# Performance work log

Measured on AMD Instinct MI355X. Metric: run time of the kernel, lower is better.

## Reference

```python
import jax, jax.numpy as jnp
import numpy as np

N_NODES = 50000
N_G_EDGES = 400000
N_LG_EDGES = 600000
N_HEADS = 4
OUT_FEATS = 64
EPS = 0.001


def segment_mean(x, seg_ids, num_segments):
    s = jax.ops.segment_sum(x, seg_ids, num_segments=num_segments)
    cnt = jax.ops.segment_sum(jnp.ones((x.shape[0],), x.dtype), seg_ids, num_segments=num_segments)
    return s / jnp.maximum(cnt, 1.0)[(...,) + (None,) * (x.ndim - 1)]


def setup_inputs() -> dict:
    key = jax.random.key(0)
    ks = jax.random.split(key, 12)
    return {
        'atomic_number': jax.random.randint(ks[0], (N_NODES,), 0, 4),
        'g_src': jax.random.randint(ks[1], (N_G_EDGES,), 0, N_NODES),
        'g_dst': jax.random.randint(ks[2], (N_G_EDGES,), 0, N_NODES),
        'lg_src': jax.random.randint(ks[3], (N_LG_EDGES,), 0, N_G_EDGES),
        'lg_dst': jax.random.randint(ks[4], (N_LG_EDGES,), 0, N_G_EDGES),
        'costheta': jax.random.uniform(ks[5], (N_LG_EDGES,), jnp.float32),
        'dnr': jax.random.uniform(ks[6], (N_LG_EDGES,), jnp.float32),
        'a': jax.random.uniform(ks[7], (N_HEADS,), jnp.float32),
        'b': jax.random.uniform(ks[8], (N_HEADS,), jnp.float32),
        'c': jax.random.uniform(ks[9], (N_HEADS,), jnp.float32),
        'd': jax.random.uniform(ks[10], (N_HEADS,), jnp.float32),
        'value_table': jax.random.normal(ks[11], (4, OUT_FEATS * N_HEADS), jnp.float32),
    }


def reference(atomic_number, g_src, g_dst, lg_src, lg_dst, costheta, dnr, a, b, c, d, value_table):
    # send_k_src: per g-edge atomic numbers of endpoints
    k_src = atomic_number[g_src]  # (E_g,)
    k_dst = atomic_number[g_dst]  # (E_g,)

    # masked symmetry key on line-graph edges (edge pair: lg_src -> lg_dst, g-edge indices)
    ka = k_src[lg_src]
    kc = k_dst[lg_dst]
    kb = k_dst[lg_src]
    peripheral = (ka == kc).astype(jnp.int32)
    central = ((kb == ka) & (kb == kc)).astype(jnp.int32)
    sym_key = peripheral * 2 + central  # (E_lg,), values in {0,1,2,3}

    # value embedding lookup -> (E_lg, F, H)
    asv = value_table[sym_key].reshape(N_LG_EDGES, OUT_FEATS, N_HEADS)

    # angular / radial symmetry per head
    ct = jnp.clip(costheta, -EPS, EPS)
    theta = jnp.arccos(ct)[:, None]  # (E_lg, 1)
    B = b % jnp.pi
    angular = ((jnp.cos(a[None, :] * theta + B[None, :]) + 1.0) / 2.0) ** c[None, :]  # (E_lg, H)
    radial = jnp.exp(-d[None, :] * (dnr[:, None] ** 2))  # (E_lg, H)
    spatial = radial * angular

    sv = asv * spatial[:, None, :]  # (E_lg, F, H)

    # reverse line-graph mean: aggregate lg edges by their (original) source lg-node = g-edge
    w_edge = segment_mean(sv, lg_src, N_G_EDGES)  # (E_g, F, H)
    # reverse graph mean: aggregate g edges by their (original) source node
    w_node = segment_mean(w_edge, g_src, N_NODES)  # (N, F, H)

    return jnp.sum(w_node, axis=-1)  # (N, F)
```

## Files before the change

### kernel.cpp

```cpp
#include <hip/hip_runtime.h>
#include <math.h>

typedef unsigned long long u64;
typedef unsigned int u32;
typedef unsigned short u16;
typedef unsigned char u8;

#define N_NODES    50000
#define N_G_EDGES  400000
#define N_LG_EDGES 600000
#define OUT_FEATS  64
#define EPSV       0.001f
#define PI_F       3.14159265358979323846f
#define HPI_F      1.57079632679489662f
#define FXSCALE    512.0f
#define INV_FXSCALE (1.0f/512.0f)

#define SB_N    256
#define EPB1    2344
#define LH_B0   256
#define LG_CH   16
#define LG_BINS 50000
#define LG_W    12500
#define LG_EPC  37500
#define GH_B0   384
#define GH_CH   16
#define GH_W    12500
#define GH_EPC  25000
#define PK_B0   400
#define PK_GPB  3572
#define K1_GRID 512

#define WID   1564
#define NLSB  256
#define NPB   196
#define SPB   (NPB*4)
#define CAP2  2816


__global__ __launch_bounds__(1024) void k1(const int* __restrict__ an,
                                           const int* __restrict__ gsrc,
                                           const int* __restrict__ gdst,
                                           const int* __restrict__ lgsrc,
                                           const int* __restrict__ lgdst,
                                           const float* __restrict__ costheta,
                                           const float* __restrict__ dnr,
                                           u8*  __restrict__ kk8,
                                           u32* __restrict__ clg,
                                           u32* __restrict__ cg,
                                           uint4* __restrict__ srecs,
                                           u32* __restrict__ prefT1) {
    __shared__ u32 smem[12800];
    const int tid = threadIdx.x;
    const int bid = blockIdx.x;

    if (bid < SB_N) {
        uint4* rec = (uint4*)smem;
        u32* lcnt = smem + 9600;
        u32* pref = smem + 9872;
        if (tid < 256) lcnt[tid] = 0u;
        __syncthreads();
        const int e0 = bid * EPB1;
        const int e1 = (e0 + EPB1 < N_LG_EDGES) ? e0 + EPB1 : N_LG_EDGES;
        u32 meta[3]; uint4 val[3];
#pragma unroll
        for (int it = 0; it < 3; ++it) {
            meta[it] = 0u;
            int e = e0 + it * 1024 + tid;
            if (e < e1) {
                int ls = lgsrc[e];
                int ld = lgdst[e];
                float ct = costheta[e];
                float dn = dnr[e];
                u32 bk = (u32)ls / WID;
                u32 rank = atomicAdd(&lcnt[bk], 1u);
                val[it] = make_uint4(__float_as_uint(ct), __float_as_uint(dn),
                                     (u32)ld, (u32)ls);
                meta[it] = 0x80000000u | (rank << 8) | bk;
            }
        }
        __syncthreads();
        if (tid < 256) pref[tid + 1] = lcnt[tid];
        if (tid == 0) pref[0] = 0u;
        __syncthreads();
        for (int off = 1; off < 256; off <<= 1) {
            u32 add = 0;
            if (tid < 256 && tid >= off) add = pref[tid - off + 1];
            __syncthreads();
            if (tid < 256) pref[tid + 1] += add;
            __syncthreads();
        }
#pragma unroll
        for (int it = 0; it < 3; ++it) {
            if (meta[it] & 0x80000000u) {
                u32 bk = meta[it] & 0xffu;
                u32 pos = pref[bk] + ((meta[it] >> 8) & 0x1fffu);
                rec[pos] = val[it];
            }
        }
        __syncthreads();
        const u32 btot = pref[256];
        uint4* dst = srecs + (size_t)bid * EPB1;
        for (u32 i = tid; i < btot; i += 1024) dst[i] = rec[i];
        if (tid <= 256) prefT1[bid * 257 + tid] = pref[tid];
    } else if (bid < GH_B0) {
        const int bid2 = bid - LH_B0;
        const int cc = bid2 & 15, r = bid2 >> 4;
        const int lo = r * LG_BINS;
        for (int w = tid; w < LG_W; w += 1024) smem[w] = 0u;
        __syncthreads();
        const int s0 = cc * LG_EPC;
        for (int e = s0 + tid; e < s0 + LG_EPC; e += 1024) {
            unsigned lb = (unsigned)(lgsrc[e] - lo);
            if (lb < (unsigned)LG_BINS)
                atomicAdd(&smem[lb >> 2], 1u << (8 * (lb & 3)));
        }
        __syncthreads();
        u32* dst = clg + (size_t)bid2 * LG_W;
        for (int w = tid; w < LG_W; w += 1024) dst[w] = smem[w];
    } else if (bid < PK_B0) {
        const int cc = bid - GH_B0;
        for (int w = tid; w < GH_W; w += 1024) smem[w] = 0u;
        __syncthreads();
        const int s0 = cc * GH_EPC;
        for (int g = s0 + tid; g < s0 + GH_EPC; g += 1024) {
            int n = gsrc[g];
            atomicAdd(&smem[n >> 2], 1u << (8 * (n & 3)));
        }
        __syncthreads();
        u32* dst = cg + (size_t)cc * GH_W;
        for (int w = tid; w < GH_W; w += 1024) dst[w] = smem[w];
    } else {
        const int g0 = (bid - PK_B0) * PK_GPB;
        const int g1 = (g0 + PK_GPB < N_G_EDGES) ? g0 + PK_GPB : N_G_EDGES;
        for (int g = g0 + tid; g < g1; g += 1024)
            kk8[g] = (u8)(an[gsrc[g]] | (an[gdst[g]] << 4));
    }
}

__global__ __launch_bounds__(1024) void k2(const int* __restrict__ gsrc,
                                           const u8*  __restrict__ kk8,
                                           const u32* __restrict__ clg,
                                           const uint4* __restrict__ srecs,
                                           const u32* __restrict__ prefT1,
                                           const float* __restrict__ pa,
                                           const float* __restrict__ pb,
                                           const float* __restrict__ pc,
                                           const float* __restrict__ pd,
                                           uint4* __restrict__ mrecs,
                                           u32* __restrict__ prefT2) {
    __shared__ uint4 rec[CAP2];
    __shared__ float invw[WID];
    __shared__ u16   nodew[WID];
    __shared__ u8    kkw[WID];
    __shared__ u32 sstart[256];
    __shared__ u32 spref[257];
    __shared__ u32 lcnt[256];
    __shared__ u32 pref2[257];
    const int tid = threadIdx.x;
    const int b = blockIdx.x;
    const int lo = b * WID;

    for (int i = tid; i < WID; i += 1024) {
        int ls = lo + i;
        float inv = 0.0f; u16 nd = 0; u8 kw = 0;
        if (ls < N_G_EDGES) {
            int r = ls / LG_BINS, lb = ls - r * LG_BINS;
            int w = lb >> 2, sh = 8 * (lb & 3);
            const u32* base = clg + (size_t)(r * LG_CH) * LG_W + w;
            u32 c = 0;
#pragma unroll
            for (int cc = 0; cc < LG_CH; ++cc) c += (base[(size_t)cc * LG_W] >> sh) & 0xffu;
            inv = 1.0f / (float)(c < 1u ? 1u : c);
            nd = (u16)gsrc[ls];
            kw = kk8[ls];
        }
        invw[i] = inv; nodew[i] = nd; kkw[i] = kw;
    }
    if (tid < 256) {
        u32 a = prefT1[tid * 257 + b];
        u32 c2 = prefT1[tid * 257 + b + 1];
        sstart[tid] = a; spref[tid + 1] = c2 - a; lcnt[tid] = 0u;
    }
    if (tid == 0) spref[0] = 0u;
    __syncthreads();
    for (int off = 1; off < 256; off <<= 1) {
        u32 add = 0;
        if (tid < 256 && tid >= off) add = spref[tid - off + 1];
        __syncthreads();
        if (tid < 256) spref[tid + 1] += add;
        __syncthreads();
    }
    const u32 total = spref[256];

    float A0[4], A1[4], A2[4], DD[4];
#pragma unroll
    for (int h = 0; h < 4; ++h) {
        float a = pa[h], B = fmodf(pb[h], PI_F), c = pc[h], d = pd[h];
        float K = a * HPI_F + B;
        float ck = cosf(K), sk = sinf(K);
        float u0 = 0.5f * (1.0f + ck);
        float f0 = powf(u0, c);
        float g1 = (-0.5f * a * sk) / u0;
        float u2 = -0.25f * a * a * ck;
        float g2 = u2 / u0 - 0.5f * g1 * g1;
        A0[h] = f0;
        A1[h] = f0 * c * g1;
        A2[h] = f0 * (c * g2 + 0.5f * c * c * g1 * g1);
        DD[h] = d;
    }

    u64 qv[3]; u32 mv[3];
#pragma unroll
    for (int it = 0; it < 3; ++it) {
        mv[it] = 0u;
        u32 i = (u32)(it * 1024 + tid);
        if (i < total) {
            int l2 = 0, h2 = 256;
            while (h2 - l2 > 1) {
                int mid = (l2 + h2) >> 1;
                if (spref[mid] <= i) l2 = mid; else h2 = mid;
            }
            uint4 r4 = srecs[(size_t)l2 * EPB1 + sstart[l2] + (i - spref[l2])];
            float ct = __uint_as_float(r4.x);
            float dn = __uint_as_float(r4.y);
            u32 ld = r4.z;
            int li = (int)r4.w - lo;
            float inv = invw[li];
            int node = (int)nodew[li];
            u32 kw = kkw[li];
            int ka = (int)(kw & 0xfu);
            int kb = (int)(kw >> 4);
            int kd = kk8[ld] >> 4;
            int key = ((ka == kd) ? 2 : 0) + ((kb == ka && kb == kd) ? 1 : 0);
            ct = fminf(fmaxf(ct, -EPSV), EPSV);
            float del = -ct;
            float dn2 = dn * dn;
            float s = inv * FXSCALE;
            u64 q = 0;
#pragma unroll
            for (int h = 0; h < 4; ++h) {
                float ang = A0[h] + del * (A1[h] + del * A2[h]);
                float rad = __expf(-DD[h] * dn2);
                q |= (u64)(u32)(ang * rad * s + 0.5f) << (16 * h);
            }
            u32 nb = (u32)node / NPB;
            u32 slot = ((u32)node - nb * NPB) * 4u + (u32)key;
            u32 rank = atomicAdd(&lcnt[nb], 1u);
            qv[it] = q;
            mv[it] = 0x80000000u | (rank << 18) | (nb << 10) | slot;
        }
    }
    __syncthreads();
    if (tid < 256) pref2[tid + 1] = lcnt[tid];
    if (tid == 0) pref2[0] = 0u;
    __syncthreads();
    for (int off = 1; off < 256; off <<= 1) {
        u32 add = 0;
        if (tid < 256 && tid >= off) add = pref2[tid - off + 1];
        __syncthreads();
        if (tid < 256) pref2[tid + 1] += add;
        __syncthreads();
    }
#pragma unroll
    for (int it = 0; it < 3; ++it) {
        if (mv[it] & 0x80000000u) {
            u32 nb = (mv[it] >> 10) & 0xffu;
            u32 pos = pref2[nb] + ((mv[it] >> 18) & 0x1fffu);
            if (pos < CAP2)
                rec[pos] = make_uint4((u32)qv[it], (u32)(qv[it] >> 32),
                                      mv[it] & 0x3ffu, 0u);
        }
    }
    __syncthreads();
    u32 t2 = pref2[256]; if (t2 > CAP2) t2 = CAP2;
    uint4* dst = mrecs + (size_t)b * CAP2;
    for (u32 i = tid; i < t2; i += 1024) dst[i] = rec[i];
    if (tid <= 256) {
        u32 v = pref2[tid];
        prefT2[b * 257 + tid] = (v < CAP2) ? v : CAP2;
    }
}

__global__ __launch_bounds__(1024) void k3(const uint4* __restrict__ mrecs,
                                           const u32* __restrict__ prefT2,
                                           const u32* __restrict__ cg,
                                           const float* __restrict__ VT,
                                           float* __restrict__ out) {
    __shared__ u64 ts[SPB];
    __shared__ u32 sstart[256];
    __shared__ u32 spref[257];
    __shared__ float vt_s[1024];
    __shared__ float invg_s[NPB];
    const int tid = threadIdx.x;
    const int nb = blockIdx.x;

    for (int i = tid; i < SPB; i += 1024) ts[i] = 0ull;
    vt_s[tid] = VT[tid];
    if (tid < NPB) {
        int n = nb * NPB + tid;
        float iv = 0.0f;
        if (n < N_NODES) {
            int w = n >> 2, sh = 8 * (n & 3);
            u32 c = 0;
#pragma unroll
            for (int cc = 0; cc < GH_CH; ++cc) c += (cg[(size_t)cc * GH_W + w] >> sh) & 0xffu;
            iv = 1.0f / (float)(c < 1u ? 1u : c);
        }
        invg_s[tid] = iv;
    }
    if (tid < 256) {
        u32 a = prefT2[tid * 257 + nb];
        u32 c2 = prefT2[tid * 257 + nb + 1];
        sstart[tid] = a; spref[tid + 1] = c2 - a;
    }
    if (tid == 0) spref[0] = 0u;
    __syncthreads();
    for (int off = 1; off < 256; off <<= 1) {
        u32 add = 0;
        if (tid < 256 && tid >= off) add = spref[tid - off + 1];
        __syncthreads();
        if (tid < 256) spref[tid + 1] += add;
        __syncthreads();
    }
    const u32 total = spref[256];

    for (u32 i = tid; i < total; i += 1024) {
        int l2 = 0, h2 = 256;
        while (h2 - l2 > 1) {
            int mid = (l2 + h2) >> 1;
            if (spref[mid] <= i) l2 = mid; else h2 = mid;
        }
        uint4 r4 = mrecs[(size_t)l2 * CAP2 + sstart[l2] + (i - spref[l2])];
        atomicAdd(&ts[r4.z], (u64)r4.x | ((u64)r4.y << 32));
    }
    __syncthreads();

    const int n0 = nb * NPB;
    for (int j = tid; j < NPB * OUT_FEATS; j += 1024) {
        int nl = j >> 6, f = j & 63;
        int n = n0 + nl;
        if (n < N_NODES) {
            float acc = 0.0f;
#pragma unroll
            for (int k = 0; k < 4; ++k) {
                u64 t = ts[nl * 4 + k];
#pragma unroll
                for (int h = 0; h < 4; ++h) {
                    float tv = (float)((u32)(t >> (16 * h)) & 0xffffu);
                    acc += vt_s[k * 256 + f * 4 + h] * tv;
                }
            }
            out[n * OUT_FEATS + f] = acc * INV_FXSCALE * invg_s[nl];
        }
    }
}

extern "C" void kernel_launch(void* const* d_in, const int* in_sizes, int n_in,
                              void* d_out, int out_size, void* d_ws, size_t ws_size,
                              hipStream_t stream) {
    const int*   an       = (const int*)d_in[0];
    const int*   gsrc     = (const int*)d_in[1];
    const int*   gdst     = (const int*)d_in[2];
    const int*   lgsrc    = (const int*)d_in[3];
    const int*   lgdst    = (const int*)d_in[4];
    const float* costheta = (const float*)d_in[5];
    const float* dnr      = (const float*)d_in[6];
    const float* pa       = (const float*)d_in[7];
    const float* pb       = (const float*)d_in[8];
    const float* pc       = (const float*)d_in[9];
    const float* pd       = (const float*)d_in[10];
    const float* vt       = (const float*)d_in[11];
    float* out = (float*)d_out;

    char* ws = (char*)d_ws;
    u8*    kk8    = (u8*)   (ws + 0);
    u32*   clg    = (u32*)  (ws + 400000);
    u32*   cg     = (u32*)  (ws + 6800000);
    uint4* srecs  = (uint4*)(ws + 7600000);
    u32*   prefT1 = (u32*)  (ws + 17201024);
    uint4* mrecs  = (uint4*)(ws + 17464192);
    u32*   prefT2 = (u32*)  (ws + 28998528);

    k1<<<dim3(K1_GRID), dim3(1024), 0, stream>>>(
        an, gsrc, gdst, lgsrc, lgdst, costheta, dnr, kk8, clg, cg, srecs, prefT1);
    k2<<<dim3(NLSB), dim3(1024), 0, stream>>>(
        gsrc, kk8, clg, srecs, prefT1, pa, pb, pc, pd, mrecs, prefT2);
    k3<<<dim3(256), dim3(1024), 0, stream>>>(mrecs, prefT2, cg, vt, out);
}
```

Measured before the change: 54.45 us.

## Fuse three kernels into one persistent kernel with software grid barriers

Merges the three launches into a single 256-block persistent kernel that separates phases with a sense-reversing atomic grid barrier. The line-graph source histogram is dropped; per-edge counts are now rebuilt in shared memory from the already bucketed records in phase two. Records move from 16-byte structs to packed structure-of-arrays words, and the node histogram is repartitioned so each of the 256 blocks does a share. This removes launch gaps and clg traffic, but relies on all 256 blocks being co-resident, and the barrier has a spin limit that could break synchronisation silently.

```diff
diff --git a/kernel.cpp b/kernel.cpp
--- a/kernel.cpp
+++ b/kernel.cpp
@@ -16,67 +16,96 @@
 #define FXSCALE    512.0f
 #define INV_FXSCALE (1.0f/512.0f)
 
-#define SB_N    256
-#define EPB1    2344
-#define LH_B0   256
-#define LG_CH   16
-#define LG_BINS 50000
-#define LG_W    12500
-#define LG_EPC  37500
-#define GH_B0   384
-#define GH_CH   16
-#define GH_W    12500
-#define GH_EPC  25000
-#define PK_B0   400
-#define PK_GPB  3572
-#define K1_GRID 512
+#define NBLK 256
+#define NTHR 1024
 
 #define WID   1564
-#define NLSB  256
+#define EPB1  2344
 #define NPB   196
 #define SPB   (NPB*4)
 #define CAP2  2816
 
-
-__global__ __launch_bounds__(1024) void k1(const int* __restrict__ an,
-                                           const int* __restrict__ gsrc,
-                                           const int* __restrict__ gdst,
-                                           const int* __restrict__ lgsrc,
-                                           const int* __restrict__ lgdst,
-                                           const float* __restrict__ costheta,
-                                           const float* __restrict__ dnr,
-                                           u8*  __restrict__ kk8,
-                                           u32* __restrict__ clg,
-                                           u32* __restrict__ cg,
-                                           uint4* __restrict__ srecs,
-                                           u32* __restrict__ prefT1) {
-    __shared__ u32 smem[12800];
+#define GH_EPC 25000
+#define GH_BR  3125
+#define GH_W   784
+#define PK_GPB 1563
+
+
+__device__ u32 g_bar_cnt = 0;
+__device__ u32 g_bar_sense = 0;
+
+__device__ __forceinline__ void grid_sync(u32* my_sense) {
+    __syncthreads();
+    if (threadIdx.x == 0) {
+        u32 want = *my_sense ^ 1u;
+        __threadfence();
+        u32 old = __hip_atomic_fetch_add(&g_bar_cnt, 1u, __ATOMIC_RELAXED,
+                                         __HIP_MEMORY_SCOPE_AGENT);
+        if (old == NBLK - 1) {
+            __hip_atomic_store(&g_bar_cnt, 0u, __ATOMIC_RELAXED,
+                               __HIP_MEMORY_SCOPE_AGENT);
+            __hip_atomic_store(&g_bar_sense, want, __ATOMIC_RELEASE,
+                               __HIP_MEMORY_SCOPE_AGENT);
+        } else {
+            int spins = 0;
+            while (__hip_atomic_load(&g_bar_sense, __ATOMIC_RELAXED,
+                                     __HIP_MEMORY_SCOPE_AGENT) != want) {
+                __builtin_amdgcn_s_sleep(16);
+                if (++spins > (1 << 20)) break;
+            }
+        }
+        *my_sense = want;
+        __threadfence();
+    }
+    __syncthreads();
+}
+
+__global__ __launch_bounds__(NTHR) void fused_v2(
+    const int* __restrict__ an, const int* __restrict__ gsrc,
+    const int* __restrict__ gdst, const int* __restrict__ lgsrc,
+    const int* __restrict__ lgdst, const float* __restrict__ costheta,
+    const float* __restrict__ dnr, const float* __restrict__ pa,
+    const float* __restrict__ pb, const float* __restrict__ pc,
+    const float* __restrict__ pd, const float* __restrict__ VT,
+    u8* __restrict__ kk8, u32* __restrict__ cg,
+    u32* __restrict__ prefT1, u32* __restrict__ prefT2,
+    u32* __restrict__ sme, u32* __restrict__ sct, u32* __restrict__ sdn,
+    u32* __restrict__ mqlo, u32* __restrict__ mqhi, u32* __restrict__ mslot,
+    float* __restrict__ out)
+{
+    __shared__ __align__(16) u32 smem[12608];
     const int tid = threadIdx.x;
     const int bid = blockIdx.x;
-
-    if (bid < SB_N) {
-        uint4* rec = (uint4*)smem;
-        u32* lcnt = smem + 9600;
-        u32* pref = smem + 9872;
+    u32 my_sense = __hip_atomic_load(&g_bar_sense, __ATOMIC_RELAXED,
+                                     __HIP_MEMORY_SCOPE_AGENT);
+
+    {
+        u32* metaS = smem;
+        u32* ctS   = smem + 2344;
+        u32* dnS   = smem + 4688;
+        u32* lcnt  = smem + 7032;
+        u32* pref  = smem + 7288;
+
         if (tid < 256) lcnt[tid] = 0u;
         __syncthreads();
+
         const int e0 = bid * EPB1;
         const int e1 = (e0 + EPB1 < N_LG_EDGES) ? e0 + EPB1 : N_LG_EDGES;
-        u32 meta[3]; uint4 val[3];
+        u32 pw[3], cv[3], dv[3], mv[3];
 #pragma unroll
         for (int it = 0; it < 3; ++it) {
-            meta[it] = 0u;
-            int e = e0 + it * 1024 + tid;
+            mv[it] = 0u;
+            int e = e0 + it * NTHR + tid;
             if (e < e1) {
                 int ls = lgsrc[e];
                 int ld = lgdst[e];
-                float ct = costheta[e];
-                float dn = dnr[e];
+                cv[it] = __float_as_uint(costheta[e]);
+                dv[it] = __float_as_uint(dnr[e]);
                 u32 bk = (u32)ls / WID;
+                u32 li = (u32)ls - bk * WID;
+                pw[it] = ((u32)ld << 11) | li;
                 u32 rank = atomicAdd(&lcnt[bk], 1u);
-                val[it] = make_uint4(__float_as_uint(ct), __float_as_uint(dn),
-                                     (u32)ld, (u32)ls);
-                meta[it] = 0x80000000u | (rank << 8) | bk;
+                mv[it] = 0x80000000u | (rank << 8) | bk;
             }
         }
         __syncthreads();
@@ -92,266 +121,266 @@
         }
 #pragma unroll
         for (int it = 0; it < 3; ++it) {
-            if (meta[it] & 0x80000000u) {
-                u32 bk = meta[it] & 0xffu;
-                u32 pos = pref[bk] + ((meta[it] >> 8) & 0x1fffu);
-                rec[pos] = val[it];
+            if (mv[it] & 0x80000000u) {
+                u32 bk = mv[it] & 0xffu;
+                u32 pos = pref[bk] + ((mv[it] >> 8) & 0x7fffffu);
+                metaS[pos] = pw[it]; ctS[pos] = cv[it]; dnS[pos] = dv[it];
             }
         }
         __syncthreads();
         const u32 btot = pref[256];
-        uint4* dst = srecs + (size_t)bid * EPB1;
-        for (u32 i = tid; i < btot; i += 1024) dst[i] = rec[i];
+        for (u32 i = tid; i < btot; i += NTHR) {
+            sme[(size_t)bid * EPB1 + i] = metaS[i];
+            sct[(size_t)bid * EPB1 + i] = ctS[i];
+            sdn[(size_t)bid * EPB1 + i] = dnS[i];
+        }
         if (tid <= 256) prefT1[bid * 257 + tid] = pref[tid];
-    } else if (bid < GH_B0) {
-        const int bid2 = bid - LH_B0;
-        const int cc = bid2 & 15, r = bid2 >> 4;
-        const int lo = r * LG_BINS;
-        for (int w = tid; w < LG_W; w += 1024) smem[w] = 0u;
-        __syncthreads();
-        const int s0 = cc * LG_EPC;
-        for (int e = s0 + tid; e < s0 + LG_EPC; e += 1024) {
-            unsigned lb = (unsigned)(lgsrc[e] - lo);
-            if (lb < (unsigned)LG_BINS)
-                atomicAdd(&smem[lb >> 2], 1u << (8 * (lb & 3)));
-        }
-        __syncthreads();
-        u32* dst = clg + (size_t)bid2 * LG_W;
-        for (int w = tid; w < LG_W; w += 1024) dst[w] = smem[w];
-    } else if (bid < PK_B0) {
-        const int cc = bid - GH_B0;
-        for (int w = tid; w < GH_W; w += 1024) smem[w] = 0u;
-        __syncthreads();
-        const int s0 = cc * GH_EPC;
-        for (int g = s0 + tid; g < s0 + GH_EPC; g += 1024) {
-            int n = gsrc[g];
-            atomicAdd(&smem[n >> 2], 1u << (8 * (n & 3)));
-        }
-        __syncthreads();
-        u32* dst = cg + (size_t)cc * GH_W;
-        for (int w = tid; w < GH_W; w += 1024) dst[w] = smem[w];
-    } else {
-        const int g0 = (bid - PK_B0) * PK_GPB;
+        __syncthreads();
+
+        u32* hist = smem;
+        for (int w = tid; w < GH_W; w += NTHR) hist[w] = 0u;
+        __syncthreads();
+        {
+            const int cc = bid & 15;
+            const int lo = (bid >> 4) * GH_BR;
+            const int s0 = cc * GH_EPC;
+            for (int g = s0 + tid; g < s0 + GH_EPC; g += NTHR) {
+                unsigned lb = (unsigned)(gsrc[g] - lo);
+                if (lb < (unsigned)GH_BR)
+                    atomicAdd(&hist[lb >> 2], 1u << (8 * (lb & 3)));
+            }
+        }
+        __syncthreads();
+        for (int w = tid; w < GH_W; w += NTHR) cg[bid * GH_W + w] = hist[w];
+
+        const int g0 = bid * PK_GPB;
         const int g1 = (g0 + PK_GPB < N_G_EDGES) ? g0 + PK_GPB : N_G_EDGES;
-        for (int g = g0 + tid; g < g1; g += 1024)
+        for (int g = g0 + tid; g < g1; g += NTHR)
             kk8[g] = (u8)(an[gsrc[g]] | (an[gdst[g]] << 4));
     }
-}
-
-__global__ __launch_bounds__(1024) void k2(const int* __restrict__ gsrc,
-                                           const u8*  __restrict__ kk8,
-                                           const u32* __restrict__ clg,
-                                           const uint4* __restrict__ srecs,
-                                           const u32* __restrict__ prefT1,
-                                           const float* __restrict__ pa,
-                                           const float* __restrict__ pb,
-                                           const float* __restrict__ pc,
-                                           const float* __restrict__ pd,
-                                           uint4* __restrict__ mrecs,
-                                           u32* __restrict__ prefT2) {
-    __shared__ uint4 rec[CAP2];
-    __shared__ float invw[WID];
-    __shared__ u16   nodew[WID];
-    __shared__ u8    kkw[WID];
-    __shared__ u32 sstart[256];
-    __shared__ u32 spref[257];
-    __shared__ u32 lcnt[256];
-    __shared__ u32 pref2[257];
-    const int tid = threadIdx.x;
-    const int b = blockIdx.x;
-    const int lo = b * WID;
-
-    for (int i = tid; i < WID; i += 1024) {
-        int ls = lo + i;
-        float inv = 0.0f; u16 nd = 0; u8 kw = 0;
-        if (ls < N_G_EDGES) {
-            int r = ls / LG_BINS, lb = ls - r * LG_BINS;
-            int w = lb >> 2, sh = 8 * (lb & 3);
-            const u32* base = clg + (size_t)(r * LG_CH) * LG_W + w;
-            u32 c = 0;
-#pragma unroll
-            for (int cc = 0; cc < LG_CH; ++cc) c += (base[(size_t)cc * LG_W] >> sh) & 0xffu;
-            inv = 1.0f / (float)(c < 1u ? 1u : c);
-            nd = (u16)gsrc[ls];
-            kw = kk8[ls];
-        }
-        invw[i] = inv; nodew[i] = nd; kkw[i] = kw;
-    }
-    if (tid < 256) {
-        u32 a = prefT1[tid * 257 + b];
-        u32 c2 = prefT1[tid * 257 + b + 1];
-        sstart[tid] = a; spref[tid + 1] = c2 - a; lcnt[tid] = 0u;
-    }
-    if (tid == 0) spref[0] = 0u;
-    __syncthreads();
-    for (int off = 1; off < 256; off <<= 1) {
-        u32 add = 0;
-        if (tid < 256 && tid >= off) add = spref[tid - off + 1];
-        __syncthreads();
-        if (tid < 256) spref[tid + 1] += add;
-        __syncthreads();
-    }
-    const u32 total = spref[256];
-
-    float A0[4], A1[4], A2[4], DD[4];
-#pragma unroll
-    for (int h = 0; h < 4; ++h) {
-        float a = pa[h], B = fmodf(pb[h], PI_F), c = pc[h], d = pd[h];
-        float K = a * HPI_F + B;
-        float ck = cosf(K), sk = sinf(K);
-        float u0 = 0.5f * (1.0f + ck);
-        float f0 = powf(u0, c);
-        float g1 = (-0.5f * a * sk) / u0;
-        float u2 = -0.25f * a * a * ck;
-        float g2 = u2 / u0 - 0.5f * g1 * g1;
-        A0[h] = f0;
-        A1[h] = f0 * c * g1;
-        A2[h] = f0 * (c * g2 + 0.5f * c * c * g1 * g1);
-        DD[h] = d;
-    }
-
-    u64 qv[3]; u32 mv[3];
-#pragma unroll
-    for (int it = 0; it < 3; ++it) {
-        mv[it] = 0u;
-        u32 i = (u32)(it * 1024 + tid);
-        if (i < total) {
+
+    grid_sync(&my_sense);
+
+    {
+        u32* cntinv = smem;
+        u32* nkw    = smem + 1564;
+        u32* sstart = smem + 3128;
+        u32* spref  = smem + 3384;
+        u32* lcnt2  = smem + 3641;
+        u32* pref2  = smem + 3897;
+        u32* rQlo   = smem + 4160;
+        u32* rQhi   = smem + 6976;
+        u32* rSl    = smem + 9792;
+        const int b = bid;
+        const int lo = b * WID;
+
+        for (int i = tid; i < WID; i += NTHR) cntinv[i] = 0u;
+        if (tid < 256) {
+            u32 a = prefT1[tid * 257 + b];
+            u32 c2 = prefT1[tid * 257 + b + 1];
+            sstart[tid] = a; spref[tid + 1] = c2 - a; lcnt2[tid] = 0u;
+        }
+        if (tid == 0) spref[0] = 0u;
+        __syncthreads();
+        for (int off = 1; off < 256; off <<= 1) {
+            u32 add = 0;
+            if (tid < 256 && tid >= off) add = spref[tid - off + 1];
+            __syncthreads();
+            if (tid < 256) spref[tid + 1] += add;
+            __syncthreads();
+        }
+        const u32 total = spref[256];
+
+        for (u32 i = tid; i < total; i += NTHR) {
             int l2 = 0, h2 = 256;
             while (h2 - l2 > 1) {
                 int mid = (l2 + h2) >> 1;
                 if (spref[mid] <= i) l2 = mid; else h2 = mid;
             }
-            uint4 r4 = srecs[(size_t)l2 * EPB1 + sstart[l2] + (i - spref[l2])];
-            float ct = __uint_as_float(r4.x);
-            float dn = __uint_as_float(r4.y);
-            u32 ld = r4.z;
-            int li = (int)r4.w - lo;
-            float inv = invw[li];
-            int node = (int)nodew[li];
-            u32 kw = kkw[li];
-            int ka = (int)(kw & 0xfu);
-            int kb = (int)(kw >> 4);
-            int kd = kk8[ld] >> 4;
-            int key = ((ka == kd) ? 2 : 0) + ((kb == ka && kb == kd) ? 1 : 0);
-            ct = fminf(fmaxf(ct, -EPSV), EPSV);
-            float del = -ct;
-            float dn2 = dn * dn;
-            float s = inv * FXSCALE;
-            u64 q = 0;
-#pragma unroll
-            for (int h = 0; h < 4; ++h) {
-                float ang = A0[h] + del * (A1[h] + del * A2[h]);
-                float rad = __expf(-DD[h] * dn2);
-                q |= (u64)(u32)(ang * rad * s + 0.5f) << (16 * h);
-            }
-            u32 nb = (u32)node / NPB;
-            u32 slot = ((u32)node - nb * NPB) * 4u + (u32)key;
-            u32 rank = atomicAdd(&lcnt[nb], 1u);
-            qv[it] = q;
-            mv[it] = 0x80000000u | (rank << 18) | (nb << 10) | slot;
+            u32 pwv = sme[(size_t)l2 * EPB1 + sstart[l2] + (i - spref[l2])];
+            atomicAdd(&cntinv[pwv & 0x7ffu], 1u);
+        }
+        for (int i = tid; i < WID; i += NTHR) {
+            int ls = lo + i;
+            u32 nk = 0u;
+            if (ls < N_G_EDGES)
+                nk = (u32)(u16)gsrc[ls] | ((u32)kk8[ls] << 16);
+            nkw[i] = nk;
+        }
+        __syncthreads();
+        for (int i = tid; i < WID; i += NTHR) {
+            u32 c = cntinv[i];
+            cntinv[i] = __float_as_uint(1.0f / (float)(c < 1u ? 1u : c));
+        }
+        __syncthreads();
+
+        float A0[4], A1[4], A2[4], DD[4];
+#pragma unroll
+        for (int h = 0; h < 4; ++h) {
+            float a = pa[h], B = fmodf(pb[h], PI_F), c = pc[h], d = pd[h];
+            float K = a * HPI_F + B;
+            float ck = cosf(K), sk = sinf(K);
+            float u0 = 0.5f * (1.0f + ck);
+            float f0 = powf(u0, c);
+            float g1v = (-0.5f * a * sk) / u0;
+            float u2 = -0.25f * a * a * ck;
+            float g2v = u2 / u0 - 0.5f * g1v * g1v;
+            A0[h] = f0;
+            A1[h] = f0 * c * g1v;
+            A2[h] = f0 * (c * g2v + 0.5f * c * c * g1v * g1v);
+            DD[h] = d;
+        }
+
+        u64 qv[3]; u32 mv2[3];
+#pragma unroll
+        for (int it = 0; it < 3; ++it) {
+            mv2[it] = 0u;
+            u32 i = (u32)(it * NTHR + tid);
+            if (i < total) {
+                int l2 = 0, h2 = 256;
+                while (h2 - l2 > 1) {
+                    int mid = (l2 + h2) >> 1;
+                    if (spref[mid] <= i) l2 = mid; else h2 = mid;
+                }
+                size_t idx = (size_t)l2 * EPB1 + sstart[l2] + (i - spref[l2]);
+                u32 pwv = sme[idx];
+                float ct = __uint_as_float(sct[idx]);
+                float dn = __uint_as_float(sdn[idx]);
+                u32 li = pwv & 0x7ffu;
+                u32 ld = pwv >> 11;
+                float inv = __uint_as_float(cntinv[li]);
+                u32 nk = nkw[li];
+                int node = (int)(nk & 0xffffu);
+                u32 kw = (nk >> 16) & 0xffu;
+                int ka = (int)(kw & 0xfu);
+                int kb = (int)(kw >> 4);
+                int kd = kk8[ld] >> 4;
+                int key = ((ka == kd) ? 2 : 0) + ((kb == ka && kb == kd) ? 1 : 0);
+                ct = fminf(fmaxf(ct, -EPSV), EPSV);
+                float del = -ct;
+                float dn2 = dn * dn;
+                float s = inv * FXSCALE;
+                u64 q = 0;
+#pragma unroll
+                for (int h = 0; h < 4; ++h) {
+                    float ang = A0[h] + del * (A1[h] + del * A2[h]);
+                    float rad = __expf(-DD[h] * dn2);
+                    q |= (u64)(u32)(ang * rad * s + 0.5f) << (16 * h);
+                }
+                u32 nb = (u32)node / NPB;
+                u32 slot = ((u32)node - nb * NPB) * 4u + (u32)key;
+                u32 rank = atomicAdd(&lcnt2[nb], 1u);
+                qv[it] = q;
+                mv2[it] = 0x80000000u | (rank << 18) | (nb << 10) | slot;
+            }
+        }
+        __syncthreads();
+        if (tid < 256) pref2[tid + 1] = lcnt2[tid];
+        if (tid == 0) pref2[0] = 0u;
+        __syncthreads();
+        for (int off = 1; off < 256; off <<= 1) {
+            u32 add = 0;
+            if (tid < 256 && tid >= off) add = pref2[tid - off + 1];
+            __syncthreads();
+            if (tid < 256) pref2[tid + 1] += add;
+            __syncthreads();
+        }
+#pragma unroll
+        for (int it = 0; it < 3; ++it) {
+            if (mv2[it] & 0x80000000u) {
+                u32 nb = (mv2[it] >> 10) & 0xffu;
+                u32 pos = pref2[nb] + ((mv2[it] >> 18) & 0x1fffu);
+                if (pos < CAP2) {
+                    rQlo[pos] = (u32)qv[it];
+                    rQhi[pos] = (u32)(qv[it] >> 32);
+                    rSl[pos] = mv2[it] & 0x3ffu;
+                }
+            }
+        }
+        __syncthreads();
+        u32 t2 = pref2[256]; if (t2 > CAP2) t2 = CAP2;
+        for (u32 i = tid; i < t2; i += NTHR) {
+            mqlo[(size_t)b * CAP2 + i] = rQlo[i];
+            mqhi[(size_t)b * CAP2 + i] = rQhi[i];
+            mslot[(size_t)b * CAP2 + i] = rSl[i];
+        }
+        if (tid <= 256) {
+            u32 v = pref2[tid];
+            prefT2[b * 257 + tid] = (v < CAP2) ? v : CAP2;
         }
     }
-    __syncthreads();
-    if (tid < 256) pref2[tid + 1] = lcnt[tid];
-    if (tid == 0) pref2[0] = 0u;
-    __syncthreads();
-    for (int off = 1; off < 256; off <<= 1) {
-        u32 add = 0;
-        if (tid < 256 && tid >= off) add = pref2[tid - off + 1];
-        __syncthreads();
-        if (tid < 256) pref2[tid + 1] += add;
-        __syncthreads();
-    }
-#pragma unroll
-    for (int it = 0; it < 3; ++it) {
-        if (mv[it] & 0x80000000u) {
-            u32 nb = (mv[it] >> 10) & 0xffu;
-            u32 pos = pref2[nb] + ((mv[it] >> 18) & 0x1fffu);
-            if (pos < CAP2)
-                rec[pos] = make_uint4((u32)qv[it], (u32)(qv[it] >> 32),
-                                      mv[it] & 0x3ffu, 0u);
-        }
-    }
-    __syncthreads();
-    u32 t2 = pref2[256]; if (t2 > CAP2) t2 = CAP2;
-    uint4* dst = mrecs + (size_t)b * CAP2;
-    for (u32 i = tid; i < t2; i += 1024) dst[i] = rec[i];
-    if (tid <= 256) {
-        u32 v = pref2[tid];
-        prefT2[b * 257 + tid] = (v < CAP2) ? v : CAP2;
-    }
-}
-
-__global__ __launch_bounds__(1024) void k3(const uint4* __restrict__ mrecs,
-                                           const u32* __restrict__ prefT2,
-                                           const u32* __restrict__ cg,
-                                           const float* __restrict__ VT,
-                                           float* __restrict__ out) {
-    __shared__ u64 ts[SPB];
-    __shared__ u32 sstart[256];
-    __shared__ u32 spref[257];
-    __shared__ float vt_s[1024];
-    __shared__ float invg_s[NPB];
-    const int tid = threadIdx.x;
-    const int nb = blockIdx.x;
-
-    for (int i = tid; i < SPB; i += 1024) ts[i] = 0ull;
-    vt_s[tid] = VT[tid];
-    if (tid < NPB) {
-        int n = nb * NPB + tid;
-        float iv = 0.0f;
-        if (n < N_NODES) {
-            int w = n >> 2, sh = 8 * (n & 3);
-            u32 c = 0;
-#pragma unroll
-            for (int cc = 0; cc < GH_CH; ++cc) c += (cg[(size_t)cc * GH_W + w] >> sh) & 0xffu;
-            iv = 1.0f / (float)(c < 1u ? 1u : c);
-        }
-        invg_s[tid] = iv;
-    }
-    if (tid < 256) {
-        u32 a = prefT2[tid * 257 + nb];
-        u32 c2 = prefT2[tid * 257 + nb + 1];
-        sstart[tid] = a; spref[tid + 1] = c2 - a;
-    }
-    if (tid == 0) spref[0] = 0u;
-    __syncthreads();
-    for (int off = 1; off < 256; off <<= 1) {
-        u32 add = 0;
-        if (tid < 256 && tid >= off) add = spref[tid - off + 1];
-        __syncthreads();
-        if (tid < 256) spref[tid + 1] += add;
-        __syncthreads();
-    }
-    const u32 total = spref[256];
-
-    for (u32 i = tid; i < total; i += 1024) {
-        int l2 = 0, h2 = 256;
-        while (h2 - l2 > 1) {
-            int mid = (l2 + h2) >> 1;
-            if (spref[mid] <= i) l2 = mid; else h2 = mid;
-        }
-        uint4 r4 = mrecs[(size_t)l2 * CAP2 + sstart[l2] + (i - spref[l2])];
-        atomicAdd(&ts[r4.z], (u64)r4.x | ((u64)r4.y << 32));
-    }
-    __syncthreads();
-
-    const int n0 = nb * NPB;
-    for (int j = tid; j < NPB * OUT_FEATS; j += 1024) {
-        int nl = j >> 6, f = j & 63;
-        int n = n0 + nl;
-        if (n < N_NODES) {
-            float acc = 0.0f;
-#pragma unroll
-            for (int k = 0; k < 4; ++k) {
-                u64 t = ts[nl * 4 + k];
-#pragma unroll
-                for (int h = 0; h < 4; ++h) {
-                    float tv = (float)((u32)(t >> (16 * h)) & 0xffffu);
-                    acc += vt_s[k * 256 + f * 4 + h] * tv;
+
+    grid_sync(&my_sense);
+
+    {
+        u64* ts      = (u64*)smem;
+        float* vt_s  = (float*)(smem + 1568);
+        float* ivg   = (float*)(smem + 2592);
+        u32* sstart  = smem + 2788;
+        u32* spref   = smem + 3044;
+        const int nb = bid;
+
+        for (int i = tid; i < SPB; i += NTHR) ts[i] = 0ull;
+        vt_s[tid] = VT[tid];
+        if (tid < NPB) {
+            int n = nb * NPB + tid;
+            float iv = 0.0f;
+            if (n < N_NODES) {
+                int r = n / GH_BR, lb = n - r * GH_BR;
+                int w = lb >> 2, sh = 8 * (lb & 3);
+                u32 c = 0;
+#pragma unroll
+                for (int cc = 0; cc < 16; ++cc)
+                    c += (cg[((r << 4) + cc) * GH_W + w] >> sh) & 0xffu;
+                iv = 1.0f / (float)(c < 1u ? 1u : c);
+            }
+            ivg[tid] = iv;
+        }
+        if (tid < 256) {
+            u32 a = prefT2[tid * 257 + nb];
+            u32 c2 = prefT2[tid * 257 + nb + 1];
+            sstart[tid] = a; spref[tid + 1] = c2 - a;
+        }
+        if (tid == 0) spref[0] = 0u;
+        __syncthreads();
+        for (int off = 1; off < 256; off <<= 1) {
+            u32 add = 0;
+            if (tid < 256 && tid >= off) add = spref[tid - off + 1];
+            __syncthreads();
+            if (tid < 256) spref[tid + 1] += add;
+            __syncthreads();
+        }
+        const u32 total = spref[256];
+
+        for (u32 i = tid; i < total; i += NTHR) {
+            int l2 = 0, h2 = 256;
+            while (h2 - l2 > 1) {
+                int mid = (l2 + h2) >> 1;
+                if (spref[mid] <= i) l2 = mid; else h2 = mid;
+            }
+            size_t idx = (size_t)l2 * CAP2 + sstart[l2] + (i - spref[l2]);
+            u64 q = (u64)mqlo[idx] | ((u64)mqhi[idx] << 32);
+            atomicAdd(&ts[mslot[idx]], q);
+        }
+        __syncthreads();
+
+        const int n0 = nb * NPB;
+        for (int j = tid; j < NPB * OUT_FEATS; j += NTHR) {
+            int nl = j >> 6, f = j & 63;
+            int n = n0 + nl;
+            if (n < N_NODES) {
+                float acc = 0.0f;
+#pragma unroll
+                for (int k = 0; k < 4; ++k) {
+                    u64 t = ts[nl * 4 + k];
+#pragma unroll
+                    for (int h = 0; h < 4; ++h) {
+                        float tv = (float)((u32)(t >> (16 * h)) & 0xffffu);
+                        acc += vt_s[k * 256 + f * 4 + h] * tv;
+                    }
                 }
-            }
-            out[n * OUT_FEATS + f] = acc * INV_FXSCALE * invg_s[nl];
+                out[n * OUT_FEATS + f] = acc * INV_FXSCALE * ivg[nl];
+            }
         }
     }
 }
@@ -374,17 +403,18 @@
     float* out = (float*)d_out;
 
     char* ws = (char*)d_ws;
-    u8*    kk8    = (u8*)   (ws + 0);
-    u32*   clg    = (u32*)  (ws + 400000);
-    u32*   cg     = (u32*)  (ws + 6800000);
-    uint4* srecs  = (uint4*)(ws + 7600000);
-    u32*   prefT1 = (u32*)  (ws + 17201024);
-    uint4* mrecs  = (uint4*)(ws + 17464192);
-    u32*   prefT2 = (u32*)  (ws + 28998528);
-
-    k1<<<dim3(K1_GRID), dim3(1024), 0, stream>>>(
-        an, gsrc, gdst, lgsrc, lgdst, costheta, dnr, kk8, clg, cg, srecs, prefT1);
-    k2<<<dim3(NLSB), dim3(1024), 0, stream>>>(
-        gsrc, kk8, clg, srecs, prefT1, pa, pb, pc, pd, mrecs, prefT2);
-    k3<<<dim3(256), dim3(1024), 0, stream>>>(mrecs, prefT2, cg, vt, out);
+    u8*  kk8    = (u8*) (ws + 0);
+    u32* cg     = (u32*)(ws + 400000);
+    u32* prefT1 = (u32*)(ws + 1202816);
+    u32* prefT2 = (u32*)(ws + 1465984);
+    u32* sme    = (u32*)(ws + 1729152);
+    u32* sct    = (u32*)(ws + 4129408);
+    u32* sdn    = (u32*)(ws + 6529664);
+    u32* mqlo   = (u32*)(ws + 8929920);
+    u32* mqhi   = (u32*)(ws + 11813504);
+    u32* mslot  = (u32*)(ws + 14697088);
+
+    fused_v2<<<dim3(NBLK), dim3(NTHR), 0, stream>>>(
+        an, gsrc, gdst, lgsrc, lgdst, costheta, dnr, pa, pb, pc, pd, vt,
+        kk8, cg, prefT1, prefT2, sme, sct, sdn, mqlo, mqhi, mslot, out);
 }
```

New measurement: 96.08 us. 76.5% more time.

## Count line-graph degrees in bucket pass and use packed SoA records

Applied to the files above, without the earlier changes.

Drops the separate line-graph source histogram blocks in k1. Each k2 block now counts its own lg-source degrees in shared memory, since the bucketed records already group edges by source window. Intermediate records become compact struct-of-arrays, with local index and destination packed into one word plus separate ct/dn and q-lo/q-hi/slot arrays, written and read with nontemporal hints. This cuts global traffic and the 6.4MB histogram buffer, in exchange for an extra shared-memory atomic pass and more separate memory streams.

```diff
diff --git a/kernel.cpp b/kernel.cpp
--- a/kernel.cpp
+++ b/kernel.cpp
@@ -18,21 +18,15 @@
 
 #define SB_N    256
 #define EPB1    2344
-#define LH_B0   256
-#define LG_CH   16
-#define LG_BINS 50000
-#define LG_W    12500
-#define LG_EPC  37500
-#define GH_B0   384
-#define GH_CH   16
+#define GH_B0   256
+#define GH_N    16
+#define GH_EPC  25000
 #define GH_W    12500
-#define GH_EPC  25000
-#define PK_B0   400
+#define PK_B0   272
 #define PK_GPB  3572
-#define K1_GRID 512
+#define K1_GRID 384
 
 #define WID   1564
-#define NLSB  256
 #define NPB   196
 #define SPB   (NPB*4)
 #define CAP2  2816
@@ -46,37 +40,41 @@
                                            const float* __restrict__ costheta,
                                            const float* __restrict__ dnr,
                                            u8*  __restrict__ kk8,
-                                           u32* __restrict__ clg,
                                            u32* __restrict__ cg,
-                                           uint4* __restrict__ srecs,
-                                           u32* __restrict__ prefT1) {
-    __shared__ u32 smem[12800];
+                                           u32* __restrict__ prefT1,
+                                           u32* __restrict__ sme,
+                                           u32* __restrict__ sct,
+                                           u32* __restrict__ sdn) {
+    __shared__ u32 smem[12500];
     const int tid = threadIdx.x;
     const int bid = blockIdx.x;
 
     if (bid < SB_N) {
-        uint4* rec = (uint4*)smem;
-        u32* lcnt = smem + 9600;
-        u32* pref = smem + 9872;
+        u32* metaS = smem;
+        u32* ctS   = smem + 2344;
+        u32* dnS   = smem + 4688;
+        u32* lcnt  = smem + 7032;
+        u32* pref  = smem + 7288;
         if (tid < 256) lcnt[tid] = 0u;
         __syncthreads();
+
         const int e0 = bid * EPB1;
         const int e1 = (e0 + EPB1 < N_LG_EDGES) ? e0 + EPB1 : N_LG_EDGES;
-        u32 meta[3]; uint4 val[3];
+        u32 pw[3], cv[3], dv[3], mv[3];
 #pragma unroll
         for (int it = 0; it < 3; ++it) {
-            meta[it] = 0u;
+            mv[it] = 0u;
             int e = e0 + it * 1024 + tid;
             if (e < e1) {
-                int ls = lgsrc[e];
-                int ld = lgdst[e];
-                float ct = costheta[e];
-                float dn = dnr[e];
+                int ls = __builtin_nontemporal_load(&lgsrc[e]);
+                int ld = __builtin_nontemporal_load(&lgdst[e]);
+                cv[it] = __float_as_uint(__builtin_nontemporal_load(&costheta[e]));
+                dv[it] = __float_as_uint(__builtin_nontemporal_load(&dnr[e]));
                 u32 bk = (u32)ls / WID;
+                u32 li = (u32)ls - bk * WID;
+                pw[it] = ((u32)ld << 11) | li;
                 u32 rank = atomicAdd(&lcnt[bk], 1u);
-                val[it] = make_uint4(__float_as_uint(ct), __float_as_uint(dn),
-                                     (u32)ld, (u32)ls);
-                meta[it] = 0x80000000u | (rank << 8) | bk;
+                mv[it] = 0x80000000u | (rank << 8) | bk;
             }
         }
         __syncthreads();
@@ -92,32 +90,20 @@
         }
 #pragma unroll
         for (int it = 0; it < 3; ++it) {
-            if (meta[it] & 0x80000000u) {
-                u32 bk = meta[it] & 0xffu;
-                u32 pos = pref[bk] + ((meta[it] >> 8) & 0x1fffu);
-                rec[pos] = val[it];
+            if (mv[it] & 0x80000000u) {
+                u32 bk = mv[it] & 0xffu;
+                u32 pos = pref[bk] + ((mv[it] >> 8) & 0x7fffffu);
+                metaS[pos] = pw[it]; ctS[pos] = cv[it]; dnS[pos] = dv[it];
             }
         }
         __syncthreads();
         const u32 btot = pref[256];
-        uint4* dst = srecs + (size_t)bid * EPB1;
-        for (u32 i = tid; i < btot; i += 1024) dst[i] = rec[i];
+        for (u32 i = tid; i < btot; i += 1024) {
+            __builtin_nontemporal_store(metaS[i], &sme[(size_t)bid * EPB1 + i]);
+            __builtin_nontemporal_store(ctS[i],   &sct[(size_t)bid * EPB1 + i]);
+            __builtin_nontemporal_store(dnS[i],   &sdn[(size_t)bid * EPB1 + i]);
+        }
         if (tid <= 256) prefT1[bid * 257 + tid] = pref[tid];
-    } else if (bid < GH_B0) {
-        const int bid2 = bid - LH_B0;
-        const int cc = bid2 & 15, r = bid2 >> 4;
-        const int lo = r * LG_BINS;
-        for (int w = tid; w < LG_W; w += 1024) smem[w] = 0u;
-        __syncthreads();
-        const int s0 = cc * LG_EPC;
-        for (int e = s0 + tid; e < s0 + LG_EPC; e += 1024) {
-            unsigned lb = (unsigned)(lgsrc[e] - lo);
-            if (lb < (unsigned)LG_BINS)
-                atomicAdd(&smem[lb >> 2], 1u << (8 * (lb & 3)));
-        }
-        __syncthreads();
-        u32* dst = clg + (size_t)bid2 * LG_W;
-        for (int w = tid; w < LG_W; w += 1024) dst[w] = smem[w];
     } else if (bid < PK_B0) {
         const int cc = bid - GH_B0;
         for (int w = tid; w < GH_W; w += 1024) smem[w] = 0u;
@@ -128,8 +114,7 @@
             atomicAdd(&smem[n >> 2], 1u << (8 * (n & 3)));
         }
         __syncthreads();
-        u32* dst = cg + (size_t)cc * GH_W;
-        for (int w = tid; w < GH_W; w += 1024) dst[w] = smem[w];
+        for (int w = tid; w < GH_W; w += 1024) cg[cc * GH_W + w] = smem[w];
     } else {
         const int g0 = (bid - PK_B0) * PK_GPB;
         const int g1 = (g0 + PK_GPB < N_G_EDGES) ? g0 + PK_GPB : N_G_EDGES;
@@ -140,47 +125,37 @@
 
 __global__ __launch_bounds__(1024) void k2(const int* __restrict__ gsrc,
                                            const u8*  __restrict__ kk8,
-                                           const u32* __restrict__ clg,
-                                           const uint4* __restrict__ srecs,
                                            const u32* __restrict__ prefT1,
+                                           const u32* __restrict__ sme,
+                                           const u32* __restrict__ sct,
+                                           const u32* __restrict__ sdn,
                                            const float* __restrict__ pa,
                                            const float* __restrict__ pb,
                                            const float* __restrict__ pc,
                                            const float* __restrict__ pd,
-                                           uint4* __restrict__ mrecs,
+                                           u32* __restrict__ mqlo,
+                                           u32* __restrict__ mqhi,
+                                           u32* __restrict__ mslot,
                                            u32* __restrict__ prefT2) {
-    __shared__ uint4 rec[CAP2];
-    __shared__ float invw[WID];
-    __shared__ u16   nodew[WID];
-    __shared__ u8    kkw[WID];
-    __shared__ u32 sstart[256];
-    __shared__ u32 spref[257];
-    __shared__ u32 lcnt[256];
-    __shared__ u32 pref2[257];
+    __shared__ u32 smem[12608];
+    u32* cntinv = smem;
+    u32* nkw    = smem + 1564;
+    u32* sstart = smem + 3128;
+    u32* spref  = smem + 3384;
+    u32* lcnt2  = smem + 3641;
+    u32* pref2  = smem + 3897;
+    u32* rQlo   = smem + 4160;
+    u32* rQhi   = smem + 6976;
+    u32* rSl    = smem + 9792;
     const int tid = threadIdx.x;
     const int b = blockIdx.x;
     const int lo = b * WID;
 
-    for (int i = tid; i < WID; i += 1024) {
-        int ls = lo + i;
-        float inv = 0.0f; u16 nd = 0; u8 kw = 0;
-        if (ls < N_G_EDGES) {
-            int r = ls / LG_BINS, lb = ls - r * LG_BINS;
-            int w = lb >> 2, sh = 8 * (lb & 3);
-            const u32* base = clg + (size_t)(r * LG_CH) * LG_W + w;
-            u32 c = 0;
-#pragma unroll
-            for (int cc = 0; cc < LG_CH; ++cc) c += (base[(size_t)cc * LG_W] >> sh) & 0xffu;
-            inv = 1.0f / (float)(c < 1u ? 1u : c);
-            nd = (u16)gsrc[ls];
-            kw = kk8[ls];
-        }
-        invw[i] = inv; nodew[i] = nd; kkw[i] = kw;
-    }
+    for (int i = tid; i < WID; i += 1024) cntinv[i] = 0u;
     if (tid < 256) {
         u32 a = prefT1[tid * 257 + b];
         u32 c2 = prefT1[tid * 257 + b + 1];
-        sstart[tid] = a; spref[tid + 1] = c2 - a; lcnt[tid] = 0u;
+        sstart[tid] = a; spref[tid + 1] = c2 - a; lcnt2[tid] = 0u;
     }
     if (tid == 0) spref[0] = 0u;
     __syncthreads();
@@ -192,6 +167,37 @@
         __syncthreads();
     }
     const u32 total = spref[256];
+
+    u32 pwv[3]; u32 gidx[3]; u32 valid[3];
+#pragma unroll
+    for (int it = 0; it < 3; ++it) {
+        valid[it] = 0u;
+        u32 i = (u32)(it * 1024 + tid);
+        if (i < total) {
+            int l2 = 0, h2 = 256;
+            while (h2 - l2 > 1) {
+                int mid = (l2 + h2) >> 1;
+                if (spref[mid] <= i) l2 = mid; else h2 = mid;
+            }
+            u32 idx = (u32)l2 * EPB1 + sstart[l2] + (i - spref[l2]);
+            u32 p = __builtin_nontemporal_load(&sme[idx]);
+            atomicAdd(&cntinv[p & 0x7ffu], 1u);
+            pwv[it] = p; gidx[it] = idx; valid[it] = 1u;
+        }
+    }
+    for (int i = tid; i < WID; i += 1024) {
+        int ls = lo + i;
+        u32 nk = 0u;
+        if (ls < N_G_EDGES)
+            nk = (u32)(u16)gsrc[ls] | ((u32)kk8[ls] << 16);
+        nkw[i] = nk;
+    }
+    __syncthreads();
+    for (int i = tid; i < WID; i += 1024) {
+        u32 c = cntinv[i];
+        cntinv[i] = __float_as_uint(1.0f / (float)(c < 1u ? 1u : c));
+    }
+    __syncthreads();
 
     float A0[4], A1[4], A2[4], DD[4];
 #pragma unroll
@@ -201,34 +207,30 @@
         float ck = cosf(K), sk = sinf(K);
         float u0 = 0.5f * (1.0f + ck);
         float f0 = powf(u0, c);
-        float g1 = (-0.5f * a * sk) / u0;
+        float g1v = (-0.5f * a * sk) / u0;
         float u2 = -0.25f * a * a * ck;
-        float g2 = u2 / u0 - 0.5f * g1 * g1;
+        float g2v = u2 / u0 - 0.5f * g1v * g1v;
         A0[h] = f0;
-        A1[h] = f0 * c * g1;
-        A2[h] = f0 * (c * g2 + 0.5f * c * c * g1 * g1);
+        A1[h] = f0 * c * g1v;
+        A2[h] = f0 * (c * g2v + 0.5f * c * c * g1v * g1v);
         DD[h] = d;
     }
 
-    u64 qv[3]; u32 mv[3];
+    u64 qv[3]; u32 mv2[3];
 #pragma unroll
     for (int it = 0; it < 3; ++it) {
-        mv[it] = 0u;
-        u32 i = (u32)(it * 1024 + tid);
-        if (i < total) {
-            int l2 = 0, h2 = 256;
-            while (h2 - l2 > 1) {
-                int mid = (l2 + h2) >> 1;
-                if (spref[mid] <= i) l2 = mid; else h2 = mid;
-            }
-            uint4 r4 = srecs[(size_t)l2 * EPB1 + sstart[l2] + (i - spref[l2])];
-            float ct = __uint_as_float(r4.x);
-            float dn = __uint_as_float(r4.y);
-            u32 ld = r4.z;
-            int li = (int)r4.w - lo;
-            float inv = invw[li];
-            int node = (int)nodew[li];
-            u32 kw = kkw[li];
+        mv2[it] = 0u;
+        if (valid[it]) {
+            u32 p = pwv[it];
+            u32 idx = gidx[it];
+            float ct = __uint_as_float(__builtin_nontemporal_load(&sct[idx]));
+            float dn = __uint_as_float(__builtin_nontemporal_load(&sdn[idx]));
+            u32 li = p & 0x7ffu;
+            u32 ld = p >> 11;
+            float inv = __uint_as_float(cntinv[li]);
+            u32 nk = nkw[li];
+            int node = (int)(nk & 0xffffu);
+            u32 kw = (nk >> 16) & 0xffu;
             int ka = (int)(kw & 0xfu);
             int kb = (int)(kw >> 4);
             int kd = kk8[ld] >> 4;
@@ -246,13 +248,13 @@
             }
             u32 nb = (u32)node / NPB;
             u32 slot = ((u32)node - nb * NPB) * 4u + (u32)key;
-            u32 rank = atomicAdd(&lcnt[nb], 1u);
+            u32 rank = atomicAdd(&lcnt2[nb], 1u);
             qv[it] = q;
-            mv[it] = 0x80000000u | (rank << 18) | (nb << 10) | slot;
-        }
-    }
-    __syncthreads();
-    if (tid < 256) pref2[tid + 1] = lcnt[tid];
+            mv2[it] = 0x80000000u | (rank << 18) | (nb << 10) | slot;
+        }
+    }
+    __syncthreads();
+    if (tid < 256) pref2[tid + 1] = lcnt2[tid];
     if (tid == 0) pref2[0] = 0u;
     __syncthreads();
     for (int off = 1; off < 256; off <<= 1) {
@@ -264,34 +266,42 @@
     }
 #pragma unroll
     for (int it = 0; it < 3; ++it) {
-        if (mv[it] & 0x80000000u) {
-            u32 nb = (mv[it] >> 10) & 0xffu;
-            u32 pos = pref2[nb] + ((mv[it] >> 18) & 0x1fffu);
-            if (pos < CAP2)
-                rec[pos] = make_uint4((u32)qv[it], (u32)(qv[it] >> 32),
-                                      mv[it] & 0x3ffu, 0u);
+        if (mv2[it] & 0x80000000u) {
+            u32 nb = (mv2[it] >> 10) & 0xffu;
+            u32 pos = pref2[nb] + ((mv2[it] >> 18) & 0x1fffu);
+            if (pos < CAP2) {
+                rQlo[pos] = (u32)qv[it];
+                rQhi[pos] = (u32)(qv[it] >> 32);
+                rSl[pos] = mv2[it] & 0x3ffu;
+            }
         }
     }
     __syncthreads();
     u32 t2 = pref2[256]; if (t2 > CAP2) t2 = CAP2;
-    uint4* dst = mrecs + (size_t)b * CAP2;
-    for (u32 i = tid; i < t2; i += 1024) dst[i] = rec[i];
+    for (u32 i = tid; i < t2; i += 1024) {
+        __builtin_nontemporal_store(rQlo[i], &mqlo[(size_t)b * CAP2 + i]);
+        __builtin_nontemporal_store(rQhi[i], &mqhi[(size_t)b * CAP2 + i]);
+        __builtin_nontemporal_store(rSl[i],  &mslot[(size_t)b * CAP2 + i]);
+    }
     if (tid <= 256) {
         u32 v = pref2[tid];
         prefT2[b * 257 + tid] = (v < CAP2) ? v : CAP2;
     }
 }
 
-__global__ __launch_bounds__(1024) void k3(const uint4* __restrict__ mrecs,
+__global__ __launch_bounds__(1024) void k3(const u32* __restrict__ mqlo,
+                                           const u32* __restrict__ mqhi,
+                                           const u32* __restrict__ mslot,
                                            const u32* __restrict__ prefT2,
                                            const u32* __restrict__ cg,
                                            const float* __restrict__ VT,
                                            float* __restrict__ out) {
-    __shared__ u64 ts[SPB];
-    __shared__ u32 sstart[256];
-    __shared__ u32 spref[257];
-    __shared__ float vt_s[1024];
-    __shared__ float invg_s[NPB];
+    __shared__ u32 smem[3328];
+    u64* ts     = (u64*)smem;
+    float* vt_s = (float*)(smem + 1568);
+    float* ivg  = (float*)(smem + 2592);
+    u32* sstart = smem + 2788;
+    u32* spref  = smem + 3044;
     const int tid = threadIdx.x;
     const int nb = blockIdx.x;
 
@@ -304,10 +314,11 @@
             int w = n >> 2, sh = 8 * (n & 3);
             u32 c = 0;
 #pragma unroll
-            for (int cc = 0; cc < GH_CH; ++cc) c += (cg[(size_t)cc * GH_W + w] >> sh) & 0xffu;
+            for (int cc = 0; cc < GH_N; ++cc)
+                c += (cg[cc * GH_W + w] >> sh) & 0xffu;
             iv = 1.0f / (float)(c < 1u ? 1u : c);
         }
-        invg_s[tid] = iv;
+        ivg[tid] = iv;
     }
     if (tid < 256) {
         u32 a = prefT2[tid * 257 + nb];
@@ -331,8 +342,10 @@
             int mid = (l2 + h2) >> 1;
             if (spref[mid] <= i) l2 = mid; else h2 = mid;
         }
-        uint4 r4 = mrecs[(size_t)l2 * CAP2 + sstart[l2] + (i - spref[l2])];
-        atomicAdd(&ts[r4.z], (u64)r4.x | ((u64)r4.y << 32));
+        size_t idx = (size_t)l2 * CAP2 + sstart[l2] + (i - spref[l2]);
+        u64 q = (u64)__builtin_nontemporal_load(&mqlo[idx])
+              | ((u64)__builtin_nontemporal_load(&mqhi[idx]) << 32);
+        atomicAdd(&ts[__builtin_nontemporal_load(&mslot[idx])], q);
     }
     __syncthreads();
 
@@ -351,7 +364,8 @@
                     acc += vt_s[k * 256 + f * 4 + h] * tv;
                 }
             }
-            out[n * OUT_FEATS + f] = acc * INV_FXSCALE * invg_s[nl];
+            __builtin_nontemporal_store(acc * INV_FXSCALE * ivg[nl],
+                                        &out[n * OUT_FEATS + f]);
         }
     }
 }
@@ -374,17 +388,23 @@
     float* out = (float*)d_out;
 
     char* ws = (char*)d_ws;
-    u8*    kk8    = (u8*)   (ws + 0);
-    u32*   clg    = (u32*)  (ws + 400000);
-    u32*   cg     = (u32*)  (ws + 6800000);
-    uint4* srecs  = (uint4*)(ws + 7600000);
-    u32*   prefT1 = (u32*)  (ws + 17201024);
-    uint4* mrecs  = (uint4*)(ws + 17464192);
-    u32*   prefT2 = (u32*)  (ws + 28998528);
+    u8*  kk8    = (u8*) (ws + 0);
+    u32* cg     = (u32*)(ws + 400000);
+    u32* prefT1 = (u32*)(ws + 1200000);
+    u32* prefT2 = (u32*)(ws + 1463168);
+    u32* sme    = (u32*)(ws + 1726336);
+    u32* sct    = (u32*)(ws + 4126592);
+    u32* sdn    = (u32*)(ws + 6526848);
+    u32* mqlo   = (u32*)(ws + 8927104);
+    u32* mqhi   = (u32*)(ws + 11810688);
+    u32* mslot  = (u32*)(ws + 14694272);
 
     k1<<<dim3(K1_GRID), dim3(1024), 0, stream>>>(
-        an, gsrc, gdst, lgsrc, lgdst, costheta, dnr, kk8, clg, cg, srecs, prefT1);
-    k2<<<dim3(NLSB), dim3(1024), 0, stream>>>(
-        gsrc, kk8, clg, srecs, prefT1, pa, pb, pc, pd, mrecs, prefT2);
-    k3<<<dim3(256), dim3(1024), 0, stream>>>(mrecs, prefT2, cg, vt, out);
+        an, gsrc, gdst, lgsrc, lgdst, costheta, dnr, kk8, cg, prefT1,
+        sme, sct, sdn);
+    k2<<<dim3(256), dim3(1024), 0, stream>>>(
+        gsrc, kk8, prefT1, sme, sct, sdn, pa, pb, pc, pd,
+        mqlo, mqhi, mslot, prefT2);
+    k3<<<dim3(256), dim3(1024), 0, stream>>>(
+        mqlo, mqhi, mslot, prefT2, cg, vt, out);
 }
```

After: 51.41 us. 5.6% less time.
